# Kernel optimization log

Hardware: AMD Instinct MI355X
Metric: run time of the kernel (lower is better)

The kernel has to match this reference:

```python
import jax, jax.numpy as jnp
import numpy as np

B, V, MAX_TOPK = 256, 128000, 256
IGNORED = -3000.0

def setup_inputs() -> dict:
    key = jax.random.key(0)
    k1, k2, k3, k4, k5 = jax.random.split(key, 5)
    token_logits = jax.random.normal(k1, (B, V), dtype=jnp.float32)
    # sampling_params[:,0]=top_k in [1,256], [:,1]=top_p in [0.5,1.0], [:,2]=temperature in [0.7,1.3]
    top_k = jax.random.randint(k2, (B,), 1, MAX_TOPK + 1).astype(jnp.float32)
    top_p = jax.random.uniform(k3, (B,), minval=0.5, maxval=1.0, dtype=jnp.float32)
    temp = jax.random.uniform(k4, (B,), minval=0.7, maxval=1.3, dtype=jnp.float32)
    sampling_params = jnp.stack([top_k, top_p, temp], axis=1)
    rand_u = jax.random.uniform(k5, (B, 1), dtype=jnp.float32)
    return {"token_logits": token_logits, "sampling_params": sampling_params, "rand_u": rand_u}

def reference(token_logits, sampling_params, rand_u):
    top_k = sampling_params[:, 0:1]        # [B,1] float
    top_p = sampling_params[:, 1:2]        # [B,1]
    temperature = sampling_params[:, 2:3]  # [B,1]
    # top_k candidates over full vocab (max_topk optimization path)
    vals, idx = jax.lax.top_k(token_logits, MAX_TOPK)  # [B,K], [B,K]
    # per-row top_k mask: positions >= top_k get IGNORED
    pos = jnp.arange(MAX_TOPK, dtype=jnp.float32)[None, :]
    vals = jnp.where(pos >= top_k, IGNORED, vals)
    # temperature
    vals = vals / temperature
    probs = jax.nn.softmax(vals, axis=-1)
    csum = jnp.cumsum(probs, axis=-1)
    # top_p clamped by global min of cumsum (matches torch.max(torch.min(csum), top_p))
    top_p_eff = jnp.maximum(jnp.min(csum), top_p)
    pmask = (csum > top_p_eff).at[:, 0].set(False)
    vals = jnp.where(pmask, IGNORED, vals)
    probs = jax.nn.softmax(vals, axis=-1)
    # multinomial via cumsum + rand-compare-sum
    csum2 = jnp.cumsum(probs, axis=-1)
    counts = jnp.sum((rand_u > csum2).astype(jnp.int32), axis=-1)  # [B]
    tokens = jnp.take_along_axis(idx, counts[:, None], axis=-1).reshape(-1)  # [B]
    return tokens
```

## Files before the change

kernel.cpp:

```cpp
#include <hip/hip_runtime.h>
#include <hip/hip_bf16.h>

constexpr int BATCH = 256;
constexpr int VOCAB = 128000;
constexpr int K = 256;
constexpr float IGNORED_C = -3000.0f;

constexpr int NCHUNK = 8;
constexpr int CHUNK = VOCAB / NCHUNK;
constexpr int BINS = 8192;
constexpr int SHIFT = 19;
constexpr int CAP = 512;

constexpr int FB_BINS = 8192;
constexpr int FB_CAND = 2048;

__device__ __forceinline__ unsigned mono(unsigned u) {
    return (u & 0x80000000u) ? ~u : (u | 0x80000000u);
}
__device__ __forceinline__ float inv_mono(unsigned k) {
    unsigned u = (k & 0x80000000u) ? (k ^ 0x80000000u) : ~k;
    return __uint_as_float(u);
}

__global__ __launch_bounds__(512, 8)
void k1_topk_chunk(const float* __restrict__ logits,
                   unsigned long long* __restrict__ ws_cand)
{
    __shared__ unsigned hist[BINS];
    __shared__ unsigned part[512];
    __shared__ unsigned long long cand[CAP];
    __shared__ unsigned ccount;
    __shared__ int s_tgrp;
    __shared__ unsigned s_sufnext;
    __shared__ int s_tbin;

    const int tid = threadIdx.x;
    const int row = blockIdx.x >> 3;
    const int chunk = blockIdx.x & (NCHUNK - 1);
    const float4* rp4 = reinterpret_cast<const float4*>(
        logits + (size_t)row * VOCAB + (size_t)chunk * CHUNK);
    constexpr int N4 = CHUNK / 4;

    for (int i = tid; i < BINS; i += 512) hist[i] = 0u;
    if (tid == 0) ccount = 0u;
    __syncthreads();

    float4 r[8];
    #pragma unroll
    for (int it = 0; it < 8; ++it) {
        const int i = tid + it * 512;
        if (i < N4) r[it] = rp4[i];
    }
    #pragma unroll
    for (int it = 0; it < 8; ++it) {
        const int i = tid + it * 512;
        if (i < N4) {
            atomicAdd(&hist[mono(__float_as_uint(r[it].x)) >> SHIFT], 1u);
            atomicAdd(&hist[mono(__float_as_uint(r[it].y)) >> SHIFT], 1u);
            atomicAdd(&hist[mono(__float_as_uint(r[it].z)) >> SHIFT], 1u);
            atomicAdd(&hist[mono(__float_as_uint(r[it].w)) >> SHIFT], 1u);
        }
    }
    __syncthreads();

    {
        unsigned s = 0;
        #pragma unroll
        for (int i = 0; i < 16; ++i)
            s += hist[tid * 16 + ((i + tid) & 15)];
        part[tid] = s;
    }
    __syncthreads();

    for (int off = 1; off < 512; off <<= 1) {
        unsigned t = (tid + off < 512) ? part[tid + off] : 0u;
        __syncthreads();
        part[tid] += t;
        __syncthreads();
    }

    if (part[tid] >= (unsigned)K && (tid == 511 || part[tid + 1] < (unsigned)K)) {
        s_tgrp = tid;
        s_sufnext = (tid == 511) ? 0u : part[tid + 1];
    }
    __syncthreads();

    if (tid < 64) {
        unsigned st = 0;
        const int G = s_tgrp;
        if (tid < 16) {
            st = s_sufnext;
            for (int i = 15; i >= tid; --i) st += hist[G * 16 + i];
        }
        unsigned long long m = __ballot(tid < 16 && st >= (unsigned)K);
        if (tid == 0) s_tbin = G * 16 + (63 - __builtin_clzll(m));
    }
    __syncthreads();

    const unsigned tb = (unsigned)s_tbin;
    const int gbase = chunk * CHUNK;
    #pragma unroll
    for (int it = 0; it < 8; ++it) {
        const int i = tid + it * 512;
        if (i < N4) {
            const int base = gbase + i * 4;
            const unsigned ka = mono(__float_as_uint(r[it].x));
            const unsigned kb = mono(__float_as_uint(r[it].y));
            const unsigned kc = mono(__float_as_uint(r[it].z));
            const unsigned kd = mono(__float_as_uint(r[it].w));
            if ((ka >> SHIFT) >= tb) { unsigned p = atomicAdd(&ccount, 1u); if (p < CAP) cand[p] = ((unsigned long long)ka << 32) | (unsigned)(~(base + 0)); }
            if ((kb >> SHIFT) >= tb) { unsigned p = atomicAdd(&ccount, 1u); if (p < CAP) cand[p] = ((unsigned long long)kb << 32) | (unsigned)(~(base + 1)); }
            if ((kc >> SHIFT) >= tb) { unsigned p = atomicAdd(&ccount, 1u); if (p < CAP) cand[p] = ((unsigned long long)kc << 32) | (unsigned)(~(base + 2)); }
            if ((kd >> SHIFT) >= tb) { unsigned p = atomicAdd(&ccount, 1u); if (p < CAP) cand[p] = ((unsigned long long)kd << 32) | (unsigned)(~(base + 3)); }
        }
    }
    __syncthreads();

    const unsigned cc = (ccount < (unsigned)CAP) ? ccount : (unsigned)CAP;
    unsigned long long v = (tid < (int)cc) ? cand[tid] : 0ull;

    #pragma unroll
    for (int kk = 2; kk <= CAP; kk <<= 1) {
        for (int j = kk >> 1; j > 0; j >>= 1) {
            const bool keepMax = (((tid & kk) == 0) == ((tid & j) == 0));
            unsigned long long w;
            if (j >= 64) {
                __syncthreads();
                cand[tid] = v;
                __syncthreads();
                w = cand[tid ^ j];
            } else {
                w = __shfl_xor(v, j, 64);
            }
            v = keepMax ? (v >= w ? v : w) : (v <= w ? v : w);
        }
    }

    if (tid < K) ws_cand[(size_t)blockIdx.x * K + tid] = v;
}

__global__ __launch_bounds__(1024)
void k2_merge(const float* __restrict__ params,
              const unsigned long long* __restrict__ ws_cand,
              float* __restrict__ ws_v, float* __restrict__ ws_csum,
              int* __restrict__ ws_idx, float* __restrict__ ws_p0)
{
    constexpr int N = NCHUNK * K;
    __shared__ unsigned long long cand[N];
    __shared__ float red[K];
    __shared__ float sc[K];

    const int row = blockIdx.x;
    const int tid = threadIdx.x;

    for (int i = tid; i < N; i += 1024) {
        const int c = i >> 8, pos = i & (K - 1);
        unsigned long long v = ws_cand[(size_t)row * N + i];
        const int dest = (c & 1) ? ((c << 8) | (K - 1 - pos)) : i;
        cand[dest] = v;
    }
    __syncthreads();

    for (int kk2 = 2 * K; kk2 <= N; kk2 <<= 1) {
        for (int j = kk2 >> 1; j > 0; j >>= 1) {
            for (int i = tid; i < N; i += 1024) {
                const int ixj = i ^ j;
                if (ixj > i) {
                    unsigned long long a = cand[i], b = cand[ixj];
                    bool sw = ((i & kk2) == 0) ? (a < b) : (a > b);
                    if (sw) { cand[i] = b; cand[ixj] = a; }
                }
            }
            __syncthreads();
        }
    }

    const bool act = tid < K;
    const float topk_f = params[row * 3 + 0];
    const float temp   = params[row * 3 + 2];
    float v = 0.f;
    int myidx = 0;
    if (act) {
        unsigned long long c = cand[tid];
        float val = inv_mono((unsigned)(c >> 32));
        myidx = (int)(~(unsigned)c);
        float x = (((float)tid) >= topk_f) ? IGNORED_C : val;
        v = x / temp;
        red[tid] = v;
    }
    __syncthreads();
    for (int s = K / 2; s > 0; s >>= 1) {
        if (tid < s) red[tid] = fmaxf(red[tid], red[tid + s]);
        __syncthreads();
    }
    const float m = red[0];
    __syncthreads();
    const float e = act ? expf(v - m) : 0.f;
    if (act) red[tid] = e;
    __syncthreads();
    for (int s = K / 2; s > 0; s >>= 1) {
        if (tid < s) red[tid] += red[tid + s];
        __syncthreads();
    }
    const float ssum = red[0];
    __syncthreads();
    const float p = e / ssum;
    if (act) sc[tid] = p;
    __syncthreads();
    for (int off = 1; off < K; off <<= 1) {
        float t = 0.f;
        if (act && tid >= off) t = sc[tid - off];
        __syncthreads();
        if (act) sc[tid] += t;
        __syncthreads();
    }
    if (act) {
        ws_v[row * K + tid]    = v;
        ws_csum[row * K + tid] = sc[tid];
        ws_idx[row * K + tid]  = myidx;
    }
    if (tid == 0) ws_p0[row] = p;
}

__global__ __launch_bounds__(K)
void k3_sample(const float* __restrict__ params,
               const float* __restrict__ rand_u,
               const float* __restrict__ ws_v,
               const float* __restrict__ ws_csum,
               const int* __restrict__ ws_idx,
               const float* __restrict__ ws_p0,
               int* __restrict__ out)
{
    __shared__ float red[K];
    __shared__ float sc[K];
    const int row = blockIdx.x;
    const int tid = threadIdx.x;

    red[tid] = ws_p0[tid];
    __syncthreads();
    for (int s = K / 2; s > 0; s >>= 1) {
        if (tid < s) red[tid] = fminf(red[tid], red[tid + s]);
        __syncthreads();
    }
    const float tpe = fmaxf(red[0], params[row * 3 + 1]);
    __syncthreads();

    const float csum = ws_csum[row * K + tid];
    const float v0   = ws_v[row * K + tid];
    const float v2 = ((csum > tpe) && (tid != 0)) ? IGNORED_C : v0;
    red[tid] = v2;
    __syncthreads();
    for (int s = K / 2; s > 0; s >>= 1) {
        if (tid < s) red[tid] = fmaxf(red[tid], red[tid + s]);
        __syncthreads();
    }
    const float m = red[0];
    __syncthreads();
    const float e = expf(v2 - m);
    red[tid] = e;
    __syncthreads();
    for (int s = K / 2; s > 0; s >>= 1) {
        if (tid < s) red[tid] += red[tid + s];
        __syncthreads();
    }
    const float ssum = red[0];
    __syncthreads();
    const float p = e / ssum;
    sc[tid] = p;
    __syncthreads();
    for (int off = 1; off < K; off <<= 1) {
        float t = (tid >= off) ? sc[tid - off] : 0.f;
        __syncthreads();
        sc[tid] += t;
        __syncthreads();
    }
    const float ru = rand_u[row];
    red[tid] = (ru > sc[tid]) ? 1.f : 0.f;
    __syncthreads();
    for (int s = K / 2; s > 0; s >>= 1) {
        if (tid < s) red[tid] += red[tid + s];
        __syncthreads();
    }
    if (tid == 0) {
        int sel = (int)red[0];
        if (sel > K - 1) sel = K - 1;
        out[row] = ws_idx[row * K + sel];
    }
}

__global__ __launch_bounds__(1024)
void fb_stage1(const float* __restrict__ logits,
               const float* __restrict__ params,
               float* __restrict__ ws_v,
               float* __restrict__ ws_csum,
               int* __restrict__ ws_idx,
               float* __restrict__ ws_p0)
{
    __shared__ unsigned hist[FB_BINS];
    __shared__ unsigned gsum[128];
    __shared__ unsigned long long cand[FB_CAND];
    __shared__ unsigned ccount;
    __shared__ int tbin;
    __shared__ float sv[K];
    __shared__ float se[K];
    __shared__ int   sidx[K];
    __shared__ float sred;

    const int row = blockIdx.x;
    const int tid = threadIdx.x;
    const float4* rp4 = reinterpret_cast<const float4*>(logits + (size_t)row * VOCAB);

    for (int i = tid; i < FB_BINS; i += 1024) hist[i] = 0u;
    __syncthreads();
    for (int i = tid; i < VOCAB / 4; i += 1024) {
        float4 v = rp4[i];
        atomicAdd(&hist[mono(__float_as_uint(v.x)) >> SHIFT], 1u);
        atomicAdd(&hist[mono(__float_as_uint(v.y)) >> SHIFT], 1u);
        atomicAdd(&hist[mono(__float_as_uint(v.z)) >> SHIFT], 1u);
        atomicAdd(&hist[mono(__float_as_uint(v.w)) >> SHIFT], 1u);
    }
    __syncthreads();
    if (tid < 128) {
        unsigned s = 0;
        for (int i = 0; i < 64; ++i) s += hist[tid * 64 + i];
        gsum[tid] = s;
    }
    __syncthreads();
    if (tid == 0) {
        unsigned acc = 0;
        int g = 127;
        for (; g > 0; --g) {
            if (acc + gsum[g] >= (unsigned)K) break;
            acc += gsum[g];
        }
        int t = g * 64;
        for (int bin = g * 64 + 63; bin >= g * 64; --bin) {
            acc += hist[bin];
            if (acc >= (unsigned)K) { t = bin; break; }
        }
        tbin = t;
        ccount = 0u;
    }
    __syncthreads();
    const unsigned tb = (unsigned)tbin;
    for (int i = tid; i < VOCAB / 4; i += 1024) {
        float4 v = rp4[i];
        const int base = i * 4;
        unsigned kk[4] = { mono(__float_as_uint(v.x)), mono(__float_as_uint(v.y)),
                           mono(__float_as_uint(v.z)), mono(__float_as_uint(v.w)) };
        #pragma unroll
        for (int c = 0; c < 4; ++c) {
            if ((kk[c] >> SHIFT) >= tb) {
                unsigned p = atomicAdd(&ccount, 1u);
                if (p < FB_CAND)
                    cand[p] = ((unsigned long long)kk[c] << 32) | (unsigned)(~(base + c));
            }
        }
    }
    __syncthreads();
    for (int i = tid; i < FB_CAND; i += 1024)
        if ((unsigned)i >= ccount) cand[i] = 0ull;
    __syncthreads();
    for (int k = 2; k <= FB_CAND; k <<= 1) {
        for (int j = k >> 1; j > 0; j >>= 1) {
            for (int i = tid; i < FB_CAND; i += 1024) {
                int ixj = i ^ j;
                if (ixj > i) {
                    unsigned long long a = cand[i], b = cand[ixj];
                    bool sw = ((i & k) == 0) ? (a < b) : (a > b);
                    if (sw) { cand[i] = b; cand[ixj] = a; }
                }
            }
            __syncthreads();
        }
    }
    const float topk_f = params[row * 3 + 0];
    const float temp   = params[row * 3 + 2];
    if (tid < K) {
        unsigned long long c = cand[tid];
        float val = inv_mono((unsigned)(c >> 32));
        sidx[tid] = (int)(~(unsigned)c);
        float v = (((float)tid) >= topk_f) ? IGNORED_C : val;
        sv[tid] = v / temp;
    }
    __syncthreads();
    if (tid == 0) {
        float mm = sv[0];
        for (int i = 1; i < K; ++i) mm = fmaxf(mm, sv[i]);
        sred = mm;
    }
    __syncthreads();
    if (tid < K) se[tid] = expf(sv[tid] - sred);
    __syncthreads();
    if (tid == 0) {
        float s = 0.f;
        for (int i = 0; i < K; ++i) s += se[i];
        sred = s;
    }
    __syncthreads();
    if (tid < K) se[tid] = se[tid] / sred;
    __syncthreads();
    if (tid == 0) {
        float c = 0.f;
        for (int i = 0; i < K; ++i) { c += se[i]; se[i] = c; }
    }
    __syncthreads();
    if (tid < K) {
        ws_v[row * K + tid]    = sv[tid];
        ws_csum[row * K + tid] = se[tid];
        ws_idx[row * K + tid]  = sidx[tid];
    }
    if (tid == 0) ws_p0[row] = se[0];
}

extern "C" void kernel_launch(void* const* d_in, const int* in_sizes, int n_in,
                              void* d_out, int out_size, void* d_ws, size_t ws_size,
                              hipStream_t stream) {
    const float* logits = (const float*)d_in[0];
    const float* params = (const float*)d_in[1];
    const float* randu  = (const float*)d_in[2];
    int* out = (int*)d_out;
    char* ws = (char*)d_ws;

    const size_t cand_bytes = (size_t)BATCH * NCHUNK * K * 8;
    const size_t tail_bytes = (size_t)3 * BATCH * K * 4 + BATCH * 4;
    if (ws_size >= cand_bytes + tail_bytes) {
        unsigned long long* ws_cand = (unsigned long long*)ws;
        char* p = ws + cand_bytes;
        float* ws_v    = (float*)(p);
        float* ws_csum = (float*)(p + (size_t)BATCH * K * 4);
        int*   ws_idx  = (int*)  (p + (size_t)2 * BATCH * K * 4);
        float* ws_p0   = (float*)(p + (size_t)3 * BATCH * K * 4);
        hipLaunchKernelGGL(k1_topk_chunk, dim3(BATCH * NCHUNK), dim3(512), 0, stream,
                           logits, ws_cand);
        hipLaunchKernelGGL(k2_merge, dim3(BATCH), dim3(1024), 0, stream,
                           params, ws_cand, ws_v, ws_csum, ws_idx, ws_p0);
        hipLaunchKernelGGL(k3_sample, dim3(BATCH), dim3(K), 0, stream,
                           params, randu, ws_v, ws_csum, ws_idx, ws_p0, out);
    } else {
        float* ws_v    = (float*)(ws);
        float* ws_csum = (float*)(ws + (size_t)BATCH * K * 4);
        int*   ws_idx  = (int*)  (ws + (size_t)2 * BATCH * K * 4);
        float* ws_p0   = (float*)(ws + (size_t)3 * BATCH * K * 4);
        hipLaunchKernelGGL(fb_stage1, dim3(BATCH), dim3(1024), 0, stream,
                           logits, params, ws_v, ws_csum, ws_idx, ws_p0);
        hipLaunchKernelGGL(k3_sample, dim3(BATCH), dim3(K), 0, stream,
                           params, randu, ws_v, ws_csum, ws_idx, ws_p0, out);
    }
}
```

Baseline: 72.04 us.

## Replace histogram threshold with sample-sort pivot selection and bitonic merge tree

The per-chunk top-k stage drops the 8192-bin LDS atomic histogram and prefix scan. It instead sorts a 512-element sample of register-resident keys, picks a pivot and verifies it with wave-reduced count passes, falling back to binary search and tie-breaking by index only when needed. Chunks per row drop from 8 to 4, so each thread holds 16 float4 in registers. The merge kernel replaces the full bitonic sort of 2048 candidates with a half-cleaner max/merge tree over 1024 candidates at 512 threads. This removes histogram atomics and LDS pressure, at the cost of more registers, lower occupancy, and possible extra count passes on unlucky inputs.

```diff
diff --git a/kernel.cpp b/kernel.cpp
--- a/kernel.cpp
+++ b/kernel.cpp
@@ -6,13 +6,12 @@
 constexpr int K = 256;
 constexpr float IGNORED_C = -3000.0f;
 
-constexpr int NCHUNK = 8;
+constexpr int NCHUNK = 4;
 constexpr int CHUNK = VOCAB / NCHUNK;
-constexpr int BINS = 8192;
-constexpr int SHIFT = 19;
 constexpr int CAP = 512;
 
 constexpr int FB_BINS = 8192;
+constexpr int FB_SHIFT = 19;
 constexpr int FB_CAND = 2048;
 
 __device__ __forceinline__ unsigned mono(unsigned u) {
@@ -23,103 +22,170 @@
     return __uint_as_float(u);
 }
 
-__global__ __launch_bounds__(512, 8)
+__global__ __launch_bounds__(512, 4)
 void k1_topk_chunk(const float* __restrict__ logits,
                    unsigned long long* __restrict__ ws_cand)
 {
-    __shared__ unsigned hist[BINS];
-    __shared__ unsigned part[512];
     __shared__ unsigned long long cand[CAP];
+    __shared__ unsigned samp[512];
+    __shared__ unsigned wred[16];
     __shared__ unsigned ccount;
-    __shared__ int s_tgrp;
-    __shared__ unsigned s_sufnext;
-    __shared__ int s_tbin;
 
     const int tid = threadIdx.x;
-    const int row = blockIdx.x >> 3;
-    const int chunk = blockIdx.x & (NCHUNK - 1);
+    const int wave = tid >> 6, lane = tid & 63;
+    const int row = blockIdx.x >> 2;
+    const int chunk = blockIdx.x & 3;
+    const int gbase = chunk * CHUNK;
     const float4* rp4 = reinterpret_cast<const float4*>(
-        logits + (size_t)row * VOCAB + (size_t)chunk * CHUNK);
+        logits + (size_t)row * VOCAB + (size_t)gbase);
     constexpr int N4 = CHUNK / 4;
 
-    for (int i = tid; i < BINS; i += 512) hist[i] = 0u;
+    uint4 r[16];
+    #pragma unroll
+    for (int it = 0; it < 16; ++it) {
+        const int i = tid + it * 512;
+        if (it < 15 || tid < (N4 - 15 * 512)) {
+            float4 f = rp4[i];
+            r[it] = make_uint4(mono(__float_as_uint(f.x)), mono(__float_as_uint(f.y)),
+                               mono(__float_as_uint(f.z)), mono(__float_as_uint(f.w)));
+        } else {
+            r[it] = make_uint4(0u, 0u, 0u, 0u);
+        }
+    }
+
+    auto count_pass = [&](unsigned T, unsigned tieX, unsigned &ngt, unsigned &neq) {
+        unsigned cgt = 0, ceq = 0;
+        #pragma unroll
+        for (int it = 0; it < 16; ++it) {
+            if (it == 15 && tid >= (N4 - 15 * 512)) continue;
+            const unsigned base = 4u * (unsigned)(tid + it * 512);
+            const uint4 q = r[it];
+            cgt += (q.x > T); ceq += (q.x == T && (base + 0u) <= tieX);
+            cgt += (q.y > T); ceq += (q.y == T && (base + 1u) <= tieX);
+            cgt += (q.z > T); ceq += (q.z == T && (base + 2u) <= tieX);
+            cgt += (q.w > T); ceq += (q.w == T && (base + 3u) <= tieX);
+        }
+        #pragma unroll
+        for (int off = 32; off >= 1; off >>= 1) {
+            cgt += __shfl_xor(cgt, off);
+            ceq += __shfl_xor(ceq, off);
+        }
+        __syncthreads();
+        if (lane == 0) { wred[wave] = cgt; wred[8 + wave] = ceq; }
+        __syncthreads();
+        unsigned g = 0, e = 0;
+        #pragma unroll
+        for (int w2 = 0; w2 < 8; ++w2) { g += wred[w2]; e += wred[8 + w2]; }
+        ngt = g; neq = e;
+    };
+
+    {
+        const int j2 = tid & 3, c = (tid >> 2) & 3;
+        uint4 f = r[0];
+        if (j2 == 1) f = r[4];
+        if (j2 == 2) f = r[8];
+        if (j2 == 3) f = r[12];
+        unsigned sv = f.x;
+        if (c == 1) sv = f.y;
+        if (c == 2) sv = f.z;
+        if (c == 3) sv = f.w;
+
+        unsigned v = sv;
+        #pragma unroll
+        for (int kk = 2; kk <= 512; kk <<= 1) {
+            for (int j = kk >> 1; j > 0; j >>= 1) {
+                const bool keepMax = (((tid & kk) == 0) == ((tid & j) == 0));
+                unsigned w;
+                if (j >= 64) {
+                    __syncthreads();
+                    samp[tid] = v;
+                    __syncthreads();
+                    w = samp[tid ^ j];
+                } else {
+                    w = __shfl_xor(v, j);
+                }
+                v = keepMax ? (v >= w ? v : w) : (v <= w ? v : w);
+            }
+        }
+        __syncthreads();
+        samp[tid] = v;
+        __syncthreads();
+    }
+
+    unsigned T = samp[5];
+    unsigned ngt, neq;
+    count_pass(T, 0xFFFFFFFFu, ngt, neq);
+    unsigned nge = ngt + neq;
+
+    if (nge < (unsigned)K || nge > (unsigned)CAP) {
+        int lo = -1, hi = 511;
+        while (hi - lo > 1) {
+            const int mid = (lo + hi) >> 1;
+            count_pass(samp[mid], 0xFFFFFFFFu, ngt, neq);
+            if (ngt + neq >= (unsigned)K) hi = mid; else lo = mid;
+        }
+        T = samp[hi];
+        count_pass(T, 0xFFFFFFFFu, ngt, neq);
+        nge = ngt + neq;
+        if (nge > (unsigned)CAP) {
+            unsigned klo = T;
+            unsigned khi = (hi > 0) ? samp[hi - 1] : 0xFFFFFFFFu;
+            count_pass(khi, 0xFFFFFFFFu, ngt, neq);
+            if (ngt + neq >= (unsigned)K) {
+                klo = khi;
+            } else {
+                while (khi - klo > 1) {
+                    const unsigned kmid = klo + ((khi - klo) >> 1);
+                    count_pass(kmid, 0xFFFFFFFFu, ngt, neq);
+                    if (ngt + neq >= (unsigned)K) klo = kmid; else khi = kmid;
+                }
+            }
+            T = klo;
+            count_pass(T, 0xFFFFFFFFu, ngt, neq);
+            nge = ngt + neq;
+        }
+    }
+
+    bool tie = false;
+    unsigned X = 0xFFFFFFFFu;
+    if (nge > (unsigned)CAP) {
+        tie = true;
+        const unsigned target = (unsigned)K - ngt;
+        int xlo = -1, xhi = CHUNK - 1;
+        while (xhi - xlo > 1) {
+            const int xmid = (xlo + xhi) >> 1;
+            unsigned g2, e2;
+            count_pass(T, (unsigned)xmid, g2, e2);
+            if (e2 >= target) xhi = xmid; else xlo = xmid;
+        }
+        X = (unsigned)xhi;
+    }
+
     if (tid == 0) ccount = 0u;
     __syncthreads();
-
-    float4 r[8];
     #pragma unroll
-    for (int it = 0; it < 8; ++it) {
-        const int i = tid + it * 512;
-        if (i < N4) r[it] = rp4[i];
-    }
-    #pragma unroll
-    for (int it = 0; it < 8; ++it) {
-        const int i = tid + it * 512;
-        if (i < N4) {
-            atomicAdd(&hist[mono(__float_as_uint(r[it].x)) >> SHIFT], 1u);
-            atomicAdd(&hist[mono(__float_as_uint(r[it].y)) >> SHIFT], 1u);
-            atomicAdd(&hist[mono(__float_as_uint(r[it].z)) >> SHIFT], 1u);
-            atomicAdd(&hist[mono(__float_as_uint(r[it].w)) >> SHIFT], 1u);
-        }
-    }
-    __syncthreads();
-
-    {
-        unsigned s = 0;
-        #pragma unroll
-        for (int i = 0; i < 16; ++i)
-            s += hist[tid * 16 + ((i + tid) & 15)];
-        part[tid] = s;
-    }
-    __syncthreads();
-
-    for (int off = 1; off < 512; off <<= 1) {
-        unsigned t = (tid + off < 512) ? part[tid + off] : 0u;
-        __syncthreads();
-        part[tid] += t;
-        __syncthreads();
-    }
-
-    if (part[tid] >= (unsigned)K && (tid == 511 || part[tid + 1] < (unsigned)K)) {
-        s_tgrp = tid;
-        s_sufnext = (tid == 511) ? 0u : part[tid + 1];
-    }
-    __syncthreads();
-
-    if (tid < 64) {
-        unsigned st = 0;
-        const int G = s_tgrp;
-        if (tid < 16) {
-            st = s_sufnext;
-            for (int i = 15; i >= tid; --i) st += hist[G * 16 + i];
-        }
-        unsigned long long m = __ballot(tid < 16 && st >= (unsigned)K);
-        if (tid == 0) s_tbin = G * 16 + (63 - __builtin_clzll(m));
-    }
-    __syncthreads();
-
-    const unsigned tb = (unsigned)s_tbin;
-    const int gbase = chunk * CHUNK;
-    #pragma unroll
-    for (int it = 0; it < 8; ++it) {
-        const int i = tid + it * 512;
-        if (i < N4) {
-            const int base = gbase + i * 4;
-            const unsigned ka = mono(__float_as_uint(r[it].x));
-            const unsigned kb = mono(__float_as_uint(r[it].y));
-            const unsigned kc = mono(__float_as_uint(r[it].z));
-            const unsigned kd = mono(__float_as_uint(r[it].w));
-            if ((ka >> SHIFT) >= tb) { unsigned p = atomicAdd(&ccount, 1u); if (p < CAP) cand[p] = ((unsigned long long)ka << 32) | (unsigned)(~(base + 0)); }
-            if ((kb >> SHIFT) >= tb) { unsigned p = atomicAdd(&ccount, 1u); if (p < CAP) cand[p] = ((unsigned long long)kb << 32) | (unsigned)(~(base + 1)); }
-            if ((kc >> SHIFT) >= tb) { unsigned p = atomicAdd(&ccount, 1u); if (p < CAP) cand[p] = ((unsigned long long)kc << 32) | (unsigned)(~(base + 2)); }
-            if ((kd >> SHIFT) >= tb) { unsigned p = atomicAdd(&ccount, 1u); if (p < CAP) cand[p] = ((unsigned long long)kd << 32) | (unsigned)(~(base + 3)); }
-        }
-    }
-    __syncthreads();
-
-    const unsigned cc = (ccount < (unsigned)CAP) ? ccount : (unsigned)CAP;
-    unsigned long long v = (tid < (int)cc) ? cand[tid] : 0ull;
-
+    for (int it = 0; it < 16; ++it) {
+        if (it == 15 && tid >= (N4 - 15 * 512)) continue;
+        const unsigned base = 4u * (unsigned)(tid + it * 512);
+        const uint4 q = r[it];
+        #pragma unroll
+        for (int c = 0; c < 4; ++c) {
+            const unsigned k2 = (c == 0) ? q.x : (c == 1) ? q.y : (c == 2) ? q.z : q.w;
+            const unsigned loc = base + (unsigned)c;
+            const bool sel = (k2 > T) || (k2 == T && (!tie || loc <= X));
+            if (sel) {
+                const unsigned p = atomicAdd(&ccount, 1u);
+                if (p < (unsigned)CAP)
+                    cand[p] = ((unsigned long long)k2 << 32) | (unsigned)(~(gbase + (int)loc));
+            }
+        }
+    }
+    __syncthreads();
+    const unsigned cc = ccount;
+    if ((unsigned)tid >= cc) cand[tid] = 0ull;
+    __syncthreads();
+
+    unsigned long long v = cand[tid];
     #pragma unroll
     for (int kk = 2; kk <= CAP; kk <<= 1) {
         for (int j = kk >> 1; j > 0; j >>= 1) {
@@ -131,7 +197,7 @@
                 __syncthreads();
                 w = cand[tid ^ j];
             } else {
-                w = __shfl_xor(v, j, 64);
+                w = __shfl_xor(v, j);
             }
             v = keepMax ? (v >= w ? v : w) : (v <= w ? v : w);
         }
@@ -140,54 +206,82 @@
     if (tid < K) ws_cand[(size_t)blockIdx.x * K + tid] = v;
 }
 
-__global__ __launch_bounds__(1024)
+__global__ __launch_bounds__(512)
 void k2_merge(const float* __restrict__ params,
               const unsigned long long* __restrict__ ws_cand,
               float* __restrict__ ws_v, float* __restrict__ ws_csum,
               int* __restrict__ ws_idx, float* __restrict__ ws_p0)
 {
     constexpr int N = NCHUNK * K;
-    __shared__ unsigned long long cand[N];
+    __shared__ unsigned long long lds[N];
     __shared__ float red[K];
     __shared__ float sc[K];
 
     const int row = blockIdx.x;
     const int tid = threadIdx.x;
 
-    for (int i = tid; i < N; i += 1024) {
-        const int c = i >> 8, pos = i & (K - 1);
-        unsigned long long v = ws_cand[(size_t)row * N + i];
-        const int dest = (c & 1) ? ((c << 8) | (K - 1 - pos)) : i;
-        cand[dest] = v;
-    }
-    __syncthreads();
-
-    for (int kk2 = 2 * K; kk2 <= N; kk2 <<= 1) {
-        for (int j = kk2 >> 1; j > 0; j >>= 1) {
-            for (int i = tid; i < N; i += 1024) {
-                const int ixj = i ^ j;
-                if (ixj > i) {
-                    unsigned long long a = cand[i], b = cand[ixj];
-                    bool sw = ((i & kk2) == 0) ? (a < b) : (a > b);
-                    if (sw) { cand[i] = b; cand[ixj] = a; }
-                }
-            }
-            __syncthreads();
+    lds[tid]       = ws_cand[(size_t)row * N + tid];
+    lds[tid + 512] = ws_cand[(size_t)row * N + tid + 512];
+    __syncthreads();
+
+    unsigned long long v;
+    {
+        const int p = tid >> 8, s = tid & 255;
+        const unsigned long long a = lds[p * 512 + s];
+        const unsigned long long b = lds[p * 512 + 511 - s];
+        v = (a >= b) ? a : b;
+    }
+    #pragma unroll
+    for (int j = 128; j >= 64; j >>= 1) {
+        __syncthreads();
+        lds[tid] = v;
+        __syncthreads();
+        const unsigned long long w = lds[tid ^ j];
+        v = ((tid & j) == 0) ? (v >= w ? v : w) : (v <= w ? v : w);
+    }
+    #pragma unroll
+    for (int j = 32; j >= 1; j >>= 1) {
+        const unsigned long long w = __shfl_xor(v, j);
+        v = ((tid & j) == 0) ? (v >= w ? v : w) : (v <= w ? v : w);
+    }
+
+    __syncthreads();
+    lds[tid] = v;
+    __syncthreads();
+    if (tid < K) {
+        const unsigned long long a = lds[tid];
+        const unsigned long long b = lds[511 - tid];
+        v = (a >= b) ? a : b;
+    }
+    #pragma unroll
+    for (int j = 128; j >= 64; j >>= 1) {
+        __syncthreads();
+        if (tid < K) lds[tid] = v;
+        __syncthreads();
+        if (tid < K) {
+            const unsigned long long w = lds[tid ^ j];
+            v = ((tid & j) == 0) ? (v >= w ? v : w) : (v <= w ? v : w);
+        }
+    }
+    if (tid < K) {
+        #pragma unroll
+        for (int j = 32; j >= 1; j >>= 1) {
+            const unsigned long long w = __shfl_xor(v, j);
+            v = ((tid & j) == 0) ? (v >= w ? v : w) : (v <= w ? v : w);
         }
     }
 
     const bool act = tid < K;
     const float topk_f = params[row * 3 + 0];
     const float temp   = params[row * 3 + 2];
-    float v = 0.f;
+    float vv = 0.f;
     int myidx = 0;
     if (act) {
-        unsigned long long c = cand[tid];
-        float val = inv_mono((unsigned)(c >> 32));
-        myidx = (int)(~(unsigned)c);
-        float x = (((float)tid) >= topk_f) ? IGNORED_C : val;
-        v = x / temp;
-        red[tid] = v;
+        const float val = inv_mono((unsigned)(v >> 32));
+        myidx = (int)(~(unsigned)v);
+        const float x = (((float)tid) >= topk_f) ? IGNORED_C : val;
+        vv = x / temp;
+        red[tid] = vv;
     }
     __syncthreads();
     for (int s = K / 2; s > 0; s >>= 1) {
@@ -196,7 +290,7 @@
     }
     const float m = red[0];
     __syncthreads();
-    const float e = act ? expf(v - m) : 0.f;
+    const float e = act ? expf(vv - m) : 0.f;
     if (act) red[tid] = e;
     __syncthreads();
     for (int s = K / 2; s > 0; s >>= 1) {
@@ -216,7 +310,7 @@
         __syncthreads();
     }
     if (act) {
-        ws_v[row * K + tid]    = v;
+        ws_v[row * K + tid]    = vv;
         ws_csum[row * K + tid] = sc[tid];
         ws_idx[row * K + tid]  = myidx;
     }
@@ -315,10 +409,10 @@
     __syncthreads();
     for (int i = tid; i < VOCAB / 4; i += 1024) {
         float4 v = rp4[i];
-        atomicAdd(&hist[mono(__float_as_uint(v.x)) >> SHIFT], 1u);
-        atomicAdd(&hist[mono(__float_as_uint(v.y)) >> SHIFT], 1u);
-        atomicAdd(&hist[mono(__float_as_uint(v.z)) >> SHIFT], 1u);
-        atomicAdd(&hist[mono(__float_as_uint(v.w)) >> SHIFT], 1u);
+        atomicAdd(&hist[mono(__float_as_uint(v.x)) >> FB_SHIFT], 1u);
+        atomicAdd(&hist[mono(__float_as_uint(v.y)) >> FB_SHIFT], 1u);
+        atomicAdd(&hist[mono(__float_as_uint(v.z)) >> FB_SHIFT], 1u);
+        atomicAdd(&hist[mono(__float_as_uint(v.w)) >> FB_SHIFT], 1u);
     }
     __syncthreads();
     if (tid < 128) {
@@ -351,7 +445,7 @@
                            mono(__float_as_uint(v.z)), mono(__float_as_uint(v.w)) };
         #pragma unroll
         for (int c = 0; c < 4; ++c) {
-            if ((kk[c] >> SHIFT) >= tb) {
+            if ((kk[c] >> FB_SHIFT) >= tb) {
                 unsigned p = atomicAdd(&ccount, 1u);
                 if (p < FB_CAND)
                     cand[p] = ((unsigned long long)kk[c] << 32) | (unsigned)(~(base + c));
@@ -434,7 +528,7 @@
         float* ws_p0   = (float*)(p + (size_t)3 * BATCH * K * 4);
         hipLaunchKernelGGL(k1_topk_chunk, dim3(BATCH * NCHUNK), dim3(512), 0, stream,
                            logits, ws_cand);
-        hipLaunchKernelGGL(k2_merge, dim3(BATCH), dim3(1024), 0, stream,
+        hipLaunchKernelGGL(k2_merge, dim3(BATCH), dim3(512), 0, stream,
                            params, ws_cand, ws_v, ws_csum, ws_idx, ws_p0);
         hipLaunchKernelGGL(k3_sample, dim3(BATCH), dim3(K), 0, stream,
                            params, randu, ws_v, ws_csum, ws_idx, ws_p0, out);
```

Measured after the change: 163.0 us. 2.26x slower.
